# Optimization experiments

Hardware: AMD Instinct MI355X
Metric: run time of the kernel (lower is better)

The kernel has to match this reference:

```python
import jax, jax.numpy as jnp
import numpy as np

H, D_IN, E = 8, 512, 512
KD = VD = E // H  # 64
B, N = 16, 1024  # batch, graph_size (== n_query, self-attention)
NEG_INF = -1e30  # stands in for -np.inf; identical post-softmax, NaN-safe


def _uniform(key, shape, stdv):
    return jax.random.uniform(key, shape, jnp.float32, -stdv, stdv)


def setup_inputs() -> dict:
    key = jax.random.key(0)
    kq, km, k1, k2, k3, k4 = jax.random.split(key, 6)
    q = jax.random.normal(kq, (B, N, D_IN), jnp.float32)
    mask = jax.random.bernoulli(km, 0.15, (B, N, N))
    W_query = _uniform(k1, (H, D_IN, KD), 1.0 / np.sqrt(KD))
    W_key = _uniform(k2, (H, D_IN, KD), 1.0 / np.sqrt(KD))
    W_val = _uniform(k3, (H, D_IN, VD), 1.0 / np.sqrt(VD))
    W_out = _uniform(k4, (H, VD, E), 1.0 / np.sqrt(E))
    return {"q": q, "mask": mask, "W_query": W_query, "W_key": W_key,
            "W_val": W_val, "W_out": W_out}


def reference(q, mask, W_query, W_key, W_val, W_out):
    # h = q (self-attention path of the module)
    kd = W_query.shape[-1]
    scale = 1.0 / np.sqrt(kd).astype(np.float32)
    Q = jnp.einsum('bni,hik->hbnk', q, W_query)   # (H,B,N,kd)
    K = jnp.einsum('bgi,hik->hbgk', q, W_key)     # (H,B,G,kd)
    V = jnp.einsum('bgi,hiv->hbgv', q, W_val)     # (H,B,G,vd)
    compat = scale * jnp.einsum('hbnk,hbgk->hbng', Q, K)  # (H,B,N,G)
    m = mask[None]                                 # (1,B,N,G) broadcasts over heads
    compat = jnp.where(m, NEG_INF, compat)
    attn = jax.nn.softmax(compat, axis=-1)
    attn = jnp.where(m, 0.0, attn)
    heads = jnp.einsum('hbng,hbgv->hbnv', attn, V)
    out = jnp.einsum('hbnv,hve->bne', heads, W_out)  # (B,N,E)
    return out
```

## Files before the change

### kernel.cpp

```cpp
#include <hip/hip_runtime.h>
#include <hip/hip_bf16.h>

#define HH 8
#define DIN 512
#define HD 64
#define BB 16
#define NN 1024
#define LOG2E 1.44269504f

typedef float f32x4 __attribute__((ext_vector_type(4)));
typedef short s16x8 __attribute__((ext_vector_type(8)));
typedef unsigned int u32x4 __attribute__((ext_vector_type(4)));
typedef __bf16 bf16x8 __attribute__((ext_vector_type(8)));

__device__ __forceinline__ short f2bf(float f) {
  union { float f; unsigned u; } v; v.f = f;
  unsigned r = v.u + 0x7FFFu + ((v.u >> 16) & 1u);
  return (short)(r >> 16);
}

__device__ __forceinline__ unsigned cvtpk(float lo, float hi) {
  unsigned r;
  asm("v_cvt_pk_bf16_f32 %0, %1, %2" : "=v"(r) : "v"(lo), "v"(hi));
  return r;
}

__device__ __forceinline__ float exp2v(float x) {
  float r;
  asm("v_exp_f32 %0, %1" : "=v"(r) : "v"(x));
  return r;
}

__device__ __forceinline__ f32x4 mfma16(s16x8 a, s16x8 b, f32x4 c) {
  return __builtin_amdgcn_mfma_f32_16x16x32_bf16(
      __builtin_bit_cast(bf16x8, a), __builtin_bit_cast(bf16x8, b), c, 0, 0, 0);
}

#define GLDS16(gsrc, ldst)                                          \
  __builtin_amdgcn_global_load_lds(                                 \
      (const __attribute__((address_space(1))) void*)(gsrc),        \
      (__attribute__((address_space(3))) void*)(ldst), 16, 0, 0)

__global__ void k_detect(const unsigned char* __restrict__ m, int* __restrict__ flag) {
  const int t = threadIdx.x;
  const int nz = (m[4 * t + 1] != 0);
  unsigned long long b = __ballot(nz);
  __shared__ unsigned int anyv;
  if (t == 0) anyv = 0u;
  __syncthreads();
  if ((t & 63) == 0 && b) atomicOr(&anyv, 1u);
  __syncthreads();
  if (t == 0) flag[0] = (int)anyv;
}

__global__ void k_packmask(const void* __restrict__ mask, const int* __restrict__ flag,
                           unsigned char* __restrict__ out) {
  const int i = blockIdx.x * 256 + threadIdx.x;
  unsigned bits = 0;
  if (flag[0]) {
    const unsigned long long v = ((const unsigned long long*)mask)[i];
#pragma unroll
    for (int j = 0; j < 8; ++j)
      bits |= (((v >> (8 * j)) & 0xFFull) ? 1u : 0u) << j;
  } else {
    const uint4 a = ((const uint4*)mask)[2 * i];
    const uint4 c = ((const uint4*)mask)[2 * i + 1];
    bits = (a.x ? 1u : 0u) | (a.y ? 2u : 0u) | (a.z ? 4u : 0u) | (a.w ? 8u : 0u) |
           (c.x ? 16u : 0u) | (c.y ? 32u : 0u) | (c.z ? 64u : 0u) | (c.w ? 128u : 0u);
  }
  out[i] = (unsigned char)bits;
}

__global__ void k_f2bf8(const float* __restrict__ src, short* __restrict__ dst, int n8) {
  const int i = blockIdx.x * 256 + threadIdx.x;
  if (i >= n8) return;
  const float4* s4 = (const float4*)src;
  float4 a = s4[2 * i], c = s4[2 * i + 1];
  s16x8 o;
  o[0] = f2bf(a.x); o[1] = f2bf(a.y); o[2] = f2bf(a.z); o[3] = f2bf(a.w);
  o[4] = f2bf(c.x); o[5] = f2bf(c.y); o[6] = f2bf(c.z); o[7] = f2bf(c.w);
  ((s16x8*)dst)[i] = o;
}

__global__ void k_wtrall(const float* __restrict__ Wq, const float* __restrict__ Wk,
                         const float* __restrict__ Wv, const float* __restrict__ Wo,
                         short* __restrict__ Wt, short* __restrict__ Wot) {
  __shared__ float t[64][65];
  const int idx = blockIdx.x;
  const float* in;
  short* op;
  int N, k0, n0;
  float scale = 1.0f;
  if (idx < 192) {
    const int mat = idx >> 6, rem = idx & 63, head = rem >> 3, kb = rem & 7;
    in = (mat == 0 ? Wq : (mat == 1 ? Wk : Wv)) + head * (DIN * HD);
    op = Wt + (size_t)(mat * 8 + head) * (HD * DIN);
    N = 64; k0 = kb * 64; n0 = 0;
    if (mat == 0) scale = 0.125f * LOG2E;
  } else {
    const int t2 = idx - 192;
    in = Wo; op = Wot;
    N = 512; k0 = (t2 >> 3) * 64; n0 = (t2 & 7) * 64;
  }
  const int tx = threadIdx.x & 63, ty = threadIdx.x >> 6;
#pragma unroll
  for (int i = 0; i < 16; ++i) {
    const int k = ty + i * 4;
    t[k][tx] = in[(size_t)(k0 + k) * N + n0 + tx];
  }
  __syncthreads();
#pragma unroll
  for (int i = 0; i < 16; ++i) {
    const int n = ty + i * 4;
    op[(size_t)(n0 + n) * DIN + k0 + tx] = f2bf(t[tx][n] * scale);
  }
}

template <int MODE>
__global__ __launch_bounds__(256, 2) void k_gemm(
    const short* __restrict__ Abf, const short* __restrict__ Bmat,
    short* __restrict__ Qb, short* __restrict__ Kb, short* __restrict__ VtG,
    float* __restrict__ out) {
  __shared__ short lds[4 * 128 * 64];
  const int tid = threadIdx.x;
  const int m0 = blockIdx.x * 128, n0 = blockIdx.y * 128;
  const int w = tid >> 6, l = tid & 63;
  const int wm = w >> 1, wn = w & 1;
  const int rowf = l & 15, kg = l >> 4;
  const int srow = l >> 3;
  const int cc = (l & 7) ^ srow;
  const bool isV = (MODE == 0) && (n0 >= 1024);

  f32x4 acc[4][4];
#pragma unroll
  for (int i = 0; i < 4; ++i)
#pragma unroll
    for (int j = 0; j < 4; ++j) acc[i][j] = (f32x4){0.f, 0.f, 0.f, 0.f};

  auto issue = [&](int kt, int bsel) {
    short* base = lds + bsel * 16384;
#pragma unroll
    for (int i = 0; i < 4; ++i) {
      const int row = w * 32 + i * 8;
      GLDS16(Abf + ((size_t)(m0 + row + srow) * 512 + kt * 64 + cc * 8),
             base + row * 64);
      GLDS16(Bmat + ((size_t)(n0 + row + srow) * 512 + kt * 64 + cc * 8),
             base + 8192 + row * 64);
    }
  };
  auto compute = [&](int bsel) {
    short* bA = lds + bsel * 16384;
    short* bB = bA + 8192;
#pragma unroll
    for (int kk = 0; kk < 2; ++kk) {
      s16x8 af[4], bf[4];
#pragma unroll
      for (int i = 0; i < 4; ++i) {
        const int arow = wm * 64 + i * 16 + rowf;
        af[i] = *(const s16x8*)&bA[arow * 64 + (((kk * 4 + kg) ^ (arow & 7)) * 8)];
        const int brow = wn * 64 + i * 16 + rowf;
        bf[i] = *(const s16x8*)&bB[brow * 64 + (((kk * 4 + kg) ^ (brow & 7)) * 8)];
      }
      if (isV) {
#pragma unroll
        for (int i = 0; i < 4; ++i)
#pragma unroll
          for (int j = 0; j < 4; ++j) acc[i][j] = mfma16(bf[j], af[i], acc[i][j]);
      } else {
#pragma unroll
        for (int i = 0; i < 4; ++i)
#pragma unroll
          for (int j = 0; j < 4; ++j) acc[i][j] = mfma16(af[i], bf[j], acc[i][j]);
      }
    }
  };

  issue(0, 0);
  issue(1, 1);
#pragma unroll 1
  for (int kt = 0; kt < 7; ++kt) {
    asm volatile("s_waitcnt vmcnt(8)" ::: "memory");
    __builtin_amdgcn_sched_barrier(0);
    __builtin_amdgcn_s_barrier();
    compute(kt & 1);
    __builtin_amdgcn_s_barrier();
    __builtin_amdgcn_sched_barrier(0);
    if (kt + 2 < 8) issue(kt + 2, kt & 1);
  }
  asm volatile("s_waitcnt vmcnt(0)" ::: "memory");
  __builtin_amdgcn_sched_barrier(0);
  __builtin_amdgcn_s_barrier();
  compute(1);

  if (MODE == 1) {
#pragma unroll
    for (int i = 0; i < 4; ++i)
#pragma unroll
      for (int j = 0; j < 4; ++j)
#pragma unroll
        for (int r = 0; r < 4; ++r) {
          const int m = m0 + wm * 64 + i * 16 + kg * 4 + r;
          const int n = n0 + wn * 64 + j * 16 + rowf;
          out[(size_t)m * DIN + n] = acc[i][j][r];
        }
  } else if (isV) {
    const int bconst = m0 >> 10;
#pragma unroll
    for (int i = 0; i < 4; ++i)
#pragma unroll
      for (int j = 0; j < 4; ++j)
#pragma unroll
        for (int r = 0; r < 4; ++r) {
          const int ng = n0 + wn * 64 + j * 16 + kg * 4 + r;
          const int head = (ng >> 6) & 7, d = ng & 63;
          const int m = m0 + wm * 64 + i * 16 + rowf;
          const int seq = m & 1023;
          VtG[((size_t)(head * BB + bconst) * HD + d) * NN + seq] = f2bf(acc[i][j][r]);
        }
  } else {
#pragma unroll
    for (int i = 0; i < 4; ++i)
#pragma unroll
      for (int j = 0; j < 4; ++j)
#pragma unroll
        for (int r = 0; r < 4; ++r) {
          const int m = m0 + wm * 64 + i * 16 + kg * 4 + r;
          const int ng = n0 + wn * 64 + j * 16 + rowf;
          const int mat = ng >> 9, head = (ng >> 6) & 7, d = ng & 63;
          short* Ob = (mat == 0 ? Qb : Kb) + head * (BB * NN * HD);
          Ob[(size_t)m * HD + d] = f2bf(acc[i][j][r]);
        }
  }
}

__global__ __launch_bounds__(512, 4) void k_attn(
    const short* __restrict__ Qb, const short* __restrict__ Kb, const short* __restrict__ VtG,
    const unsigned int* __restrict__ mw, short* __restrict__ heads) {
  __shared__ short smem[2 * 9216];
  const int tid = threadIdx.x;
  const int w = tid >> 6, l = tid & 63, rowf = l & 15, kg = l >> 4;
  const int lin = blockIdx.x;
  const int gi = (lin >> 3) + ((lin & 7) << 6);
  const int qblk = gi & 3, bh = gi >> 2;
  const int b = bh & 15, h = bh >> 4;
  const int hb = (h * BB + b) * NN;
  const short* Qp = Qb + (size_t)hb * HD;
  const short* Kp = Kb + (size_t)hb * HD;
  const short* Vtp = VtG + (size_t)(h * BB + b) * HD * NN;
  const int wq = qblk * 256 + w * 32;

  s16x8 bQ[2][2];
#pragma unroll
  for (int qi = 0; qi < 2; ++qi)
#pragma unroll
    for (int kk = 0; kk < 2; ++kk)
      bQ[qi][kk] = *(const s16x8*)&Qp[(wq + qi * 16 + rowf) * HD + kk * 32 + kg * 8];

  const f32x4 cW = (f32x4){-24.f, -24.f, -24.f, -24.f};
  f32x4 accO[2][4], accSum[2];
#pragma unroll
  for (int qi = 0; qi < 2; ++qi) {
    accSum[qi] = (f32x4){0.f, 0.f, 0.f, 0.f};
#pragma unroll
    for (int vj = 0; vj < 4; ++vj) accO[qi][vj] = (f32x4){0.f, 0.f, 0.f, 0.f};
  }
  s16x8 aOnes;
#pragma unroll
  for (int jj = 0; jj < 8; ++jj) aOnes[jj] = (short)0x3F80;

  const int kr = tid >> 3, c8 = (tid & 7) * 8;
  const int mK = ((kr >> 5) << 1) | ((kr >> 2) & 1);
  const int iK = (((kr >> 3) & 3) << 2) | (kr & 3);
  const int dK = (mK * 16 + iK) * 72 + c8;
  const int dV = 4608 + kr * 72 + c8;

  s16x8 rk = *(const s16x8*)&Kp[kr * HD + c8];
  s16x8 rv = *(const s16x8*)&Vtp[(size_t)kr * NN + c8];
  *(s16x8*)&smem[dK] = rk;
  *(s16x8*)&smem[dV] = rv;
  rk = *(const s16x8*)&Kp[(64 + kr) * HD + c8];
  rv = *(const s16x8*)&Vtp[(size_t)kr * NN + 64 + c8];

  const unsigned int* mrow0 = mw + (size_t)(b * NN + wq + rowf) * 32;

  int cur = 0;
  for (int kt = 0; kt < NN / 64; ++kt) {
    __syncthreads();
    short* bK = smem + cur * 9216;
    short* bV = bK + 4608;
    if (kt + 1 < NN / 64) {
      short* oB = smem + (cur ^ 1) * 9216;
      *(s16x8*)&oB[dK] = rk;
      *(s16x8*)&oB[dV] = rv;
      if (kt + 2 < NN / 64) {
        const int kn = (kt + 2) * 64;
        rk = *(const s16x8*)&Kp[(kn + kr) * HD + c8];
        rv = *(const s16x8*)&Vtp[(size_t)kr * NN + kn + c8];
      }
    }

    f32x4 accS[2][4];
    __builtin_amdgcn_s_setprio(1);
#pragma unroll
    for (int m = 0; m < 4; ++m) {
      s16x8 a0 = *(const s16x8*)&bK[(m * 16 + rowf) * 72 + kg * 8];
      s16x8 a1 = *(const s16x8*)&bK[(m * 16 + rowf) * 72 + 32 + kg * 8];
      accS[0][m] = mfma16(a0, bQ[0][0], cW);
      accS[0][m] = mfma16(a1, bQ[0][1], accS[0][m]);
      accS[1][m] = mfma16(a0, bQ[1][0], cW);
      accS[1][m] = mfma16(a1, bQ[1][1], accS[1][m]);
    }
    __builtin_amdgcn_s_setprio(0);

    u32x4 pw[2][2];
#pragma unroll
    for (int qi = 0; qi < 2; ++qi) {
      const uint2 mv = *(const uint2*)(mrow0 + qi * 512 + kt * 2);
      const unsigned u0 = mv.x >> (kg * 8);
      const unsigned u1 = mv.y >> (kg * 8);
#pragma unroll
      for (int half = 0; half < 2; ++half) {
        const unsigned u = half ? u1 : u0;
        u32x4 wd;
#pragma unroll
        for (int t = 0; t < 4; ++t) {
          const int j0 = 2 * t, j1 = 2 * t + 1;
          const float e0 = ((u >> j0) & 1u) ? 0.f
                           : exp2v(accS[qi][half * 2 + (j0 >> 2)][j0 & 3]);
          const float e1 = ((u >> j1) & 1u) ? 0.f
                           : exp2v(accS[qi][half * 2 + (j1 >> 2)][j1 & 3]);
          wd[t] = cvtpk(e0, e1);
        }
        pw[qi][half] = wd;
      }
    }

    __builtin_amdgcn_s_setprio(1);
#pragma unroll
    for (int kk = 0; kk < 2; ++kk) {
      const s16x8 pa0 = __builtin_bit_cast(s16x8, pw[0][kk]);
      const s16x8 pa1 = __builtin_bit_cast(s16x8, pw[1][kk]);
      accSum[0] = mfma16(aOnes, pa0, accSum[0]);
      accSum[1] = mfma16(aOnes, pa1, accSum[1]);
#pragma unroll
      for (int vj = 0; vj < 4; ++vj) {
        s16x8 aV = *(const s16x8*)&bV[(vj * 16 + rowf) * 72 + kk * 32 + kg * 8];
        accO[0][vj] = mfma16(aV, pa0, accO[0][vj]);
        accO[1][vj] = mfma16(aV, pa1, accO[1][vj]);
      }
    }
    __builtin_amdgcn_s_setprio(0);
    cur ^= 1;
  }

  __syncthreads();
  short* tb = smem + w * 2304;
  {
    const float rc0 = 1.0f / accSum[0][0], rc1 = 1.0f / accSum[1][0];
#pragma unroll
    for (int qi = 0; qi < 2; ++qi) {
      const float rc = qi ? rc1 : rc0;
#pragma unroll
      for (int vj = 0; vj < 4; ++vj)
#pragma unroll
        for (int r = 0; r < 4; ++r)
          tb[(qi * 16 + rowf) * 72 + vj * 16 + kg * 4 + r] = f2bf(accO[qi][vj][r] * rc);
    }
  }
#pragma unroll
  for (int it = 0; it < 4; ++it) {
    const int ql = (l >> 3) + it * 8, oct = l & 7;
    s16x8 v = *(const s16x8*)&tb[ql * 72 + oct * 8];
    *(s16x8*)&heads[((size_t)(b * NN + wq + ql) * HH + h) * HD + oct * 8] = v;
  }
}

extern "C" void kernel_launch(void* const* d_in, const int* in_sizes, int n_in,
                              void* d_out, int out_size, void* d_ws, size_t ws_size,
                              hipStream_t stream) {
  if (n_in < 6) return;
  const float* q  = (const float*)d_in[0];
  const void*  mk = d_in[1];
  const float* Wq = (const float*)d_in[2];
  const float* Wk = (const float*)d_in[3];
  const float* Wv = (const float*)d_in[4];
  const float* Wo = (const float*)d_in[5];
  float* out = (float*)d_out;

  char* ws = (char*)d_ws;
  size_t o = 0;
  auto alloc = [&](size_t sz) { char* p = ws + o; o = (o + sz + 255) & ~(size_t)255; return p; };
  int*           flag   = (int*)alloc(4);
  unsigned char* mwords = (unsigned char*)alloc((size_t)BB * NN * NN / 8);
  short* qbf   = (short*)alloc((size_t)BB * NN * DIN * 2);
  short* Wt    = (short*)alloc((size_t)3 * HH * HD * DIN * 2);
  short* Wot   = (short*)alloc((size_t)DIN * DIN * 2);
  short* Qbuf  = (short*)alloc((size_t)HH * BB * NN * HD * 2);
  short* Kbuf  = (short*)alloc((size_t)HH * BB * NN * HD * 2);
  short* VtBuf = (short*)alloc((size_t)HH * BB * HD * NN * 2);
  short* heads = (short*)alloc((size_t)BB * NN * HH * HD * 2);
  if (o > ws_size) return;

  k_detect<<<1, 256, 0, stream>>>((const unsigned char*)mk, flag);
  k_packmask<<<(BB * NN * NN / 8) / 256, 256, 0, stream>>>(mk, flag, mwords);
  k_f2bf8<<<(BB * NN * DIN / 8) / 256, 256, 0, stream>>>(q, qbf, BB * NN * DIN / 8);
  k_wtrall<<<256, 256, 0, stream>>>(Wq, Wk, Wv, Wo, Wt, Wot);
  k_gemm<0><<<dim3(BB * NN / 128, 12), 256, 0, stream>>>(
      qbf, Wt, Qbuf, Kbuf, VtBuf, nullptr);
  k_attn<<<dim3(512), 512, 0, stream>>>(Qbuf, Kbuf, VtBuf,
                                        (const unsigned int*)mwords, heads);
  k_gemm<1><<<dim3(BB * NN / 128, 4), 256, 0, stream>>>(
      heads, Wot, nullptr, nullptr, nullptr, out);
}
```

Before: 122.5 us.

## Merge prep kernels into one launch and XOR-swizzle attention LDS tiles

The mask packing, q-to-bf16 conversion and weight transposes are folded into a single k_prep launch with block-range dispatch, cutting two kernel launches and the gaps between them. Separately, the attention kernel's K/V and output staging tiles in shared memory move from 72-element padded rows to unpadded 64-element rows with an XOR swizzle on 16-byte chunks. This is meant to avoid LDS bank conflicts while shrinking shared memory per block. The merged kernel allocates the 64x65 float tile in every block, and the swizzle adds a little index arithmetic.

```diff
diff --git a/kernel.cpp b/kernel.cpp
--- a/kernel.cpp
+++ b/kernel.cpp
@@ -53,66 +53,66 @@
   if (t == 0) flag[0] = (int)anyv;
 }
 
-__global__ void k_packmask(const void* __restrict__ mask, const int* __restrict__ flag,
-                           unsigned char* __restrict__ out) {
-  const int i = blockIdx.x * 256 + threadIdx.x;
-  unsigned bits = 0;
-  if (flag[0]) {
-    const unsigned long long v = ((const unsigned long long*)mask)[i];
-#pragma unroll
-    for (int j = 0; j < 8; ++j)
-      bits |= (((v >> (8 * j)) & 0xFFull) ? 1u : 0u) << j;
+__global__ void k_prep(const void* __restrict__ mk, const int* __restrict__ flag,
+                       unsigned char* __restrict__ mwords,
+                       const float* __restrict__ q, short* __restrict__ qbf,
+                       const float* __restrict__ Wq, const float* __restrict__ Wk,
+                       const float* __restrict__ Wv, const float* __restrict__ Wo,
+                       short* __restrict__ Wt, short* __restrict__ Wot) {
+  __shared__ float t[64][65];
+  const int blk = blockIdx.x;
+  if (blk < 8192) {
+    const int i = blk * 256 + threadIdx.x;
+    unsigned bits = 0;
+    if (flag[0]) {
+      const unsigned long long v = ((const unsigned long long*)mk)[i];
+#pragma unroll
+      for (int j = 0; j < 8; ++j)
+        bits |= (((v >> (8 * j)) & 0xFFull) ? 1u : 0u) << j;
+    } else {
+      const uint4 a = ((const uint4*)mk)[2 * i];
+      const uint4 c = ((const uint4*)mk)[2 * i + 1];
+      bits = (a.x ? 1u : 0u) | (a.y ? 2u : 0u) | (a.z ? 4u : 0u) | (a.w ? 8u : 0u) |
+             (c.x ? 16u : 0u) | (c.y ? 32u : 0u) | (c.z ? 64u : 0u) | (c.w ? 128u : 0u);
+    }
+    mwords[i] = (unsigned char)bits;
+  } else if (blk < 12288) {
+    const int i = (blk - 8192) * 256 + threadIdx.x;
+    const float4* s4 = (const float4*)q;
+    float4 a = s4[2 * i], c = s4[2 * i + 1];
+    s16x8 o;
+    o[0] = f2bf(a.x); o[1] = f2bf(a.y); o[2] = f2bf(a.z); o[3] = f2bf(a.w);
+    o[4] = f2bf(c.x); o[5] = f2bf(c.y); o[6] = f2bf(c.z); o[7] = f2bf(c.w);
+    ((s16x8*)qbf)[i] = o;
   } else {
-    const uint4 a = ((const uint4*)mask)[2 * i];
-    const uint4 c = ((const uint4*)mask)[2 * i + 1];
-    bits = (a.x ? 1u : 0u) | (a.y ? 2u : 0u) | (a.z ? 4u : 0u) | (a.w ? 8u : 0u) |
-           (c.x ? 16u : 0u) | (c.y ? 32u : 0u) | (c.z ? 64u : 0u) | (c.w ? 128u : 0u);
-  }
-  out[i] = (unsigned char)bits;
-}
-
-__global__ void k_f2bf8(const float* __restrict__ src, short* __restrict__ dst, int n8) {
-  const int i = blockIdx.x * 256 + threadIdx.x;
-  if (i >= n8) return;
-  const float4* s4 = (const float4*)src;
-  float4 a = s4[2 * i], c = s4[2 * i + 1];
-  s16x8 o;
-  o[0] = f2bf(a.x); o[1] = f2bf(a.y); o[2] = f2bf(a.z); o[3] = f2bf(a.w);
-  o[4] = f2bf(c.x); o[5] = f2bf(c.y); o[6] = f2bf(c.z); o[7] = f2bf(c.w);
-  ((s16x8*)dst)[i] = o;
-}
-
-__global__ void k_wtrall(const float* __restrict__ Wq, const float* __restrict__ Wk,
-                         const float* __restrict__ Wv, const float* __restrict__ Wo,
-                         short* __restrict__ Wt, short* __restrict__ Wot) {
-  __shared__ float t[64][65];
-  const int idx = blockIdx.x;
-  const float* in;
-  short* op;
-  int N, k0, n0;
-  float scale = 1.0f;
-  if (idx < 192) {
-    const int mat = idx >> 6, rem = idx & 63, head = rem >> 3, kb = rem & 7;
-    in = (mat == 0 ? Wq : (mat == 1 ? Wk : Wv)) + head * (DIN * HD);
-    op = Wt + (size_t)(mat * 8 + head) * (HD * DIN);
-    N = 64; k0 = kb * 64; n0 = 0;
-    if (mat == 0) scale = 0.125f * LOG2E;
-  } else {
-    const int t2 = idx - 192;
-    in = Wo; op = Wot;
-    N = 512; k0 = (t2 >> 3) * 64; n0 = (t2 & 7) * 64;
-  }
-  const int tx = threadIdx.x & 63, ty = threadIdx.x >> 6;
-#pragma unroll
-  for (int i = 0; i < 16; ++i) {
-    const int k = ty + i * 4;
-    t[k][tx] = in[(size_t)(k0 + k) * N + n0 + tx];
-  }
-  __syncthreads();
-#pragma unroll
-  for (int i = 0; i < 16; ++i) {
-    const int n = ty + i * 4;
-    op[(size_t)(n0 + n) * DIN + k0 + tx] = f2bf(t[tx][n] * scale);
+    const int idx = blk - 12288;
+    const float* in;
+    short* op;
+    int N, k0, n0;
+    float scale = 1.0f;
+    if (idx < 192) {
+      const int mat = idx >> 6, rem = idx & 63, head = rem >> 3, kb = rem & 7;
+      in = (mat == 0 ? Wq : (mat == 1 ? Wk : Wv)) + head * (DIN * HD);
+      op = Wt + (size_t)(mat * 8 + head) * (HD * DIN);
+      N = 64; k0 = kb * 64; n0 = 0;
+      if (mat == 0) scale = 0.125f * LOG2E;
+    } else {
+      const int t2 = idx - 192;
+      in = Wo; op = Wot;
+      N = 512; k0 = (t2 >> 3) * 64; n0 = (t2 & 7) * 64;
+    }
+    const int tx = threadIdx.x & 63, ty = threadIdx.x >> 6;
+#pragma unroll
+    for (int i = 0; i < 16; ++i) {
+      const int k = ty + i * 4;
+      t[k][tx] = in[(size_t)(k0 + k) * N + n0 + tx];
+    }
+    __syncthreads();
+#pragma unroll
+    for (int i = 0; i < 16; ++i) {
+      const int n = ty + i * 4;
+      op[(size_t)(n0 + n) * DIN + k0 + tx] = f2bf(t[tx][n] * scale);
+    }
   }
 }
 
@@ -236,9 +236,10 @@
 __global__ __launch_bounds__(512, 4) void k_attn(
     const short* __restrict__ Qb, const short* __restrict__ Kb, const short* __restrict__ VtG,
     const unsigned int* __restrict__ mw, short* __restrict__ heads) {
-  __shared__ short smem[2 * 9216];
+  __shared__ short smem[2 * 8192];
   const int tid = threadIdx.x;
   const int w = tid >> 6, l = tid & 63, rowf = l & 15, kg = l >> 4;
+  const int r7 = rowf & 7;
   const int lin = blockIdx.x;
   const int gi = (lin >> 3) + ((lin & 7) << 6);
   const int qblk = gi & 3, bh = gi >> 2;
@@ -268,34 +269,35 @@
 #pragma unroll
   for (int jj = 0; jj < 8; ++jj) aOnes[jj] = (short)0x3F80;
 
-  const int kr = tid >> 3, c8 = (tid & 7) * 8;
+  const int kr = tid >> 3, c = tid & 7;
   const int mK = ((kr >> 5) << 1) | ((kr >> 2) & 1);
   const int iK = (((kr >> 3) & 3) << 2) | (kr & 3);
-  const int dK = (mK * 16 + iK) * 72 + c8;
-  const int dV = 4608 + kr * 72 + c8;
-
-  s16x8 rk = *(const s16x8*)&Kp[kr * HD + c8];
-  s16x8 rv = *(const s16x8*)&Vtp[(size_t)kr * NN + c8];
+  const int RK = mK * 16 + iK;
+  const int dK = RK * 64 + ((c ^ (RK & 7)) * 8);
+  const int dV = 4096 + kr * 64 + ((c ^ (kr & 7)) * 8);
+
+  s16x8 rk = *(const s16x8*)&Kp[kr * HD + c * 8];
+  s16x8 rv = *(const s16x8*)&Vtp[(size_t)kr * NN + c * 8];
   *(s16x8*)&smem[dK] = rk;
   *(s16x8*)&smem[dV] = rv;
-  rk = *(const s16x8*)&Kp[(64 + kr) * HD + c8];
-  rv = *(const s16x8*)&Vtp[(size_t)kr * NN + 64 + c8];
+  rk = *(const s16x8*)&Kp[(64 + kr) * HD + c * 8];
+  rv = *(const s16x8*)&Vtp[(size_t)kr * NN + 64 + c * 8];
 
   const unsigned int* mrow0 = mw + (size_t)(b * NN + wq + rowf) * 32;
 
   int cur = 0;
   for (int kt = 0; kt < NN / 64; ++kt) {
     __syncthreads();
-    short* bK = smem + cur * 9216;
-    short* bV = bK + 4608;
+    short* bK = smem + cur * 8192;
+    short* bV = bK + 4096;
     if (kt + 1 < NN / 64) {
-      short* oB = smem + (cur ^ 1) * 9216;
+      short* oB = smem + (cur ^ 1) * 8192;
       *(s16x8*)&oB[dK] = rk;
       *(s16x8*)&oB[dV] = rv;
       if (kt + 2 < NN / 64) {
         const int kn = (kt + 2) * 64;
-        rk = *(const s16x8*)&Kp[(kn + kr) * HD + c8];
-        rv = *(const s16x8*)&Vtp[(size_t)kr * NN + kn + c8];
+        rk = *(const s16x8*)&Kp[(kn + kr) * HD + c * 8];
+        rv = *(const s16x8*)&Vtp[(size_t)kr * NN + kn + c * 8];
       }
     }
 
@@ -303,8 +305,9 @@
     __builtin_amdgcn_s_setprio(1);
 #pragma unroll
     for (int m = 0; m < 4; ++m) {
-      s16x8 a0 = *(const s16x8*)&bK[(m * 16 + rowf) * 72 + kg * 8];
-      s16x8 a1 = *(const s16x8*)&bK[(m * 16 + rowf) * 72 + 32 + kg * 8];
+      const int R = m * 16 + rowf;
+      s16x8 a0 = *(const s16x8*)&bK[R * 64 + ((kg ^ r7) * 8)];
+      s16x8 a1 = *(const s16x8*)&bK[R * 64 + (((4 + kg) ^ r7) * 8)];
       accS[0][m] = mfma16(a0, bQ[0][0], cW);
       accS[0][m] = mfma16(a1, bQ[0][1], accS[0][m]);
       accS[1][m] = mfma16(a0, bQ[1][0], cW);
@@ -344,7 +347,8 @@
       accSum[1] = mfma16(aOnes, pa1, accSum[1]);
 #pragma unroll
       for (int vj = 0; vj < 4; ++vj) {
-        s16x8 aV = *(const s16x8*)&bV[(vj * 16 + rowf) * 72 + kk * 32 + kg * 8];
+        const int d = vj * 16 + rowf;
+        s16x8 aV = *(const s16x8*)&bV[d * 64 + (((kk * 4 + kg) ^ r7) * 8)];
         accO[0][vj] = mfma16(aV, pa0, accO[0][vj]);
         accO[1][vj] = mfma16(aV, pa1, accO[1][vj]);
       }
@@ -354,23 +358,27 @@
   }
 
   __syncthreads();
-  short* tb = smem + w * 2304;
+  short* tb = smem + w * 2048;
   {
     const float rc0 = 1.0f / accSum[0][0], rc1 = 1.0f / accSum[1][0];
 #pragma unroll
     for (int qi = 0; qi < 2; ++qi) {
       const float rc = qi ? rc1 : rc0;
+      const int row = qi * 16 + rowf;
 #pragma unroll
       for (int vj = 0; vj < 4; ++vj)
 #pragma unroll
-        for (int r = 0; r < 4; ++r)
-          tb[(qi * 16 + rowf) * 72 + vj * 16 + kg * 4 + r] = f2bf(accO[qi][vj][r] * rc);
+        for (int r = 0; r < 4; ++r) {
+          const int col = vj * 16 + kg * 4 + r;
+          tb[row * 64 + (((col >> 3) ^ (row & 7)) * 8) + (col & 7)] =
+              f2bf(accO[qi][vj][r] * rc);
+        }
     }
   }
 #pragma unroll
   for (int it = 0; it < 4; ++it) {
     const int ql = (l >> 3) + it * 8, oct = l & 7;
-    s16x8 v = *(const s16x8*)&tb[ql * 72 + oct * 8];
+    s16x8 v = *(const s16x8*)&tb[ql * 64 + ((oct ^ (ql & 7)) * 8)];
     *(s16x8*)&heads[((size_t)(b * NN + wq + ql) * HH + h) * HD + oct * 8] = v;
   }
 }
@@ -402,9 +410,7 @@
   if (o > ws_size) return;
 
   k_detect<<<1, 256, 0, stream>>>((const unsigned char*)mk, flag);
-  k_packmask<<<(BB * NN * NN / 8) / 256, 256, 0, stream>>>(mk, flag, mwords);
-  k_f2bf8<<<(BB * NN * DIN / 8) / 256, 256, 0, stream>>>(q, qbf, BB * NN * DIN / 8);
-  k_wtrall<<<256, 256, 0, stream>>>(Wq, Wk, Wv, Wo, Wt, Wot);
+  k_prep<<<12544, 256, 0, stream>>>(mk, flag, mwords, q, qbf, Wq, Wk, Wv, Wo, Wt, Wot);
   k_gemm<0><<<dim3(BB * NN / 128, 12), 256, 0, stream>>>(
       qbf, Wt, Qbuf, Kbuf, VtBuf, nullptr);
   k_attn<<<dim3(512), 512, 0, stream>>>(Qbuf, Kbuf, VtBuf,
```

New measurement: 118.3 us. 3.4% less time.
